# Kernel optimization log

Hardware: AMD Instinct MI355X
Metric: run time of the kernel (lower is better)

Reference implementation:

```python
import jax, jax.numpy as jnp
import numpy as np

TEMP = 5.0      # torch_kmeans SoftKMeans default temperature
N_ITERS = 25    # fixed iteration count (tolerance-based stop removed for jit)
EPS = 1e-9


def _soft_kmeans(x, l, key):
    # x: (r, q, d) -> labels (r, q) int32, centers (r, l, d)
    r, q, d = x.shape
    keys = jax.random.split(key, r)
    # random-point init (one permutation per batch, first l points)
    idx = jax.vmap(lambda k: jax.random.permutation(k, q)[:l])(keys)  # (r, l)
    centers = jnp.take_along_axis(x, idx[:, :, None], axis=1)         # (r, l, d)
    x_sq = jnp.sum(x * x, axis=-1)                                    # (r, q)

    def dist_to(centers):
        # squared euclidean distance (r, q, l)
        return (x_sq[:, :, None]
                - 2.0 * jnp.einsum('rqd,rld->rql', x, centers)
                + jnp.sum(centers * centers, axis=-1)[:, None, :])

    def step(centers, _):
        w = jax.nn.softmax(-TEMP * dist_to(centers), axis=-1)         # (r, q, l)
        denom = jnp.sum(w, axis=1)[:, :, None] + EPS                  # (r, l, 1)
        centers = jnp.einsum('rql,rqd->rld', w, x) / denom
        return centers, None

    centers, _ = jax.lax.scan(step, centers, None, length=N_ITERS)
    labels = jnp.argmin(dist_to(centers), axis=-1)                    # (r, q)
    return labels, centers


def setup_inputs() -> dict:
    key = jax.random.key(0)
    x = jax.random.normal(key, (8, 2048, 1024), dtype=jnp.float32)
    return {"x": x, "q": 4096, "r": 8, "l": 256}


def reference(x, q, r, l):
    B, T, F = x.shape
    # B*T*F must equal r*q*d; mirrors x.view(B,-1).view(B,q,-1).view(r,q,-1)
    xr = x.reshape(r, q, -1)
    labels, centers = _soft_kmeans(xr, l, jax.random.key(42))
    # gather centroid per point: rec[b, i, :] = centers[b, labels[b, i], :]
    rec = jnp.take_along_axis(centers, labels[:, :, None], axis=1)    # (r, q, d)
    return rec.reshape(B, T, F)
```

## Files before the change

kernel.cpp:

```cpp
#include <hip/hip_runtime.h>
#include <stdint.h>

#define RB 8
#define QN 4096
#define DN 512
#define LN 256
#define NITERS 25

typedef double f64x4 __attribute__((ext_vector_type(4)));

__device__ __forceinline__ void tf2x32(uint32_t k0, uint32_t k1,
                                       uint32_t x0, uint32_t x1,
                                       uint32_t& y0, uint32_t& y1) {
  uint32_t ks2 = k0 ^ k1 ^ 0x1BD11BDAu;
#define TFR(r) { x0 += x1; x1 = (x1 << (r)) | (x1 >> (32 - (r))); x1 ^= x0; }
  x0 += k0; x1 += k1;
  TFR(13) TFR(15) TFR(26) TFR(6)   x0 += k1;  x1 += ks2 + 1u;
  TFR(17) TFR(29) TFR(16) TFR(24)  x0 += ks2; x1 += k0 + 2u;
  TFR(13) TFR(15) TFR(26) TFR(6)   x0 += k0;  x1 += k1 + 3u;
  TFR(17) TFR(29) TFR(16) TFR(24)  x0 += k1;  x1 += ks2 + 4u;
  TFR(13) TFR(15) TFR(26) TFR(6)   x0 += ks2; x1 += k0 + 5u;
#undef TFR
  y0 = x0; y1 = x1;
}
// ... 79 lines not shown
  f64x4 acc = {0.0, 0.0, 0.0, 0.0};
#pragma unroll
  for (int kk = 0; kk < 4; kk++) {
    double a  = xT[kk * 4 + kg][li];
    double bv = cT[kk * 4 + kg][li];
    acc = __builtin_amdgcn_mfma_f64_16x16x4f64(a, bv, acc, 0, 0, 0);
  }
  bool ok1 = true, ok2 = true;
#pragma unroll
  for (int d = 0; d < 4; d++) {
    int q1 = kg * 4 + d;
    int q2 = kg + 4 * d;
    double ref1 = 0.0, ref2 = 0.0;
    for (int dd = 0; dd < 16; dd++) {
      ref1 += xT[dd][q1] * cT[dd][li];
      ref2 += xT[dd][q2] * cT[dd][li];
    }
    ok1 = ok1 && (acc[d] == ref1);
    ok2 = ok2 && (acc[d] == ref2);
  }
  unsigned long long v1 = __ballot(ok1);
  unsigned long long v2 = __ballot(ok2);
  if (t == 0) *flag = (v1 == ~0ull) ? 1 : ((v2 == ~0ull) ? 2 : 0);
}

#define QT 64
#define XPD 69
#define CPD 261
#define DK 16
#define XLD 82
#define CLDf 260
__device__ __forceinline__ int grow(int q) { return q + ((q >> 3) << 1); }

#define ARENA_D 5920

__global__ __launch_bounds__(256, 2) void k_assign(const float* __restrict__ x,
                                                   const float* __restrict__ centers,
                                                   const double* __restrict__ csqd,
                                                   float* __restrict__ W,
                                                   const int* __restrict__ flag) {
  __shared__ double arena[ARENA_D];
  const int mode = *flag;
  const int b = blockIdx.y, q0 = blockIdx.x * QT, t = threadIdx.x;
  const float* xb = x + ((size_t)b * QN + q0) * DN;
  const float* cb = centers + (size_t)b * LN * DN;
  const int xrow = t >> 2, xc4 = t & 3;

  if (mode != 0) {
    double (*xT)[XPD]  = (double(*)[XPD])arena;
    double (*cT)[CPD]  = (double(*)[CPD])(arena + 16 * XPD);
    double (*redm)[5]  = (double(*)[5])(arena + 16 * XPD + 16 * CPD);
    double (*reds)[5]  = (double(*)[5])(arena + 16 * XPD + 16 * CPD + 320);
    const int w = t >> 6, lane = t & 63;
    const int kg = lane >> 4, li = lane & 15;

    f64x4 acc[4][4];
#pragma unroll
    for (int i = 0; i < 4; i++)
#pragma unroll
      for (int j = 0; j < 4; j++) acc[i][j] = (f64x4){0.0, 0.0, 0.0, 0.0};

    float4 gx, gc[4];
    gx = *(const float4*)(xb + (size_t)xrow * DN + xc4 * 4);
#pragma unroll
    for (int i = 0; i < 4; i++) {
      int f = t + 256 * i; int row = f >> 2, c4 = f & 3;
      gc[i] = *(const float4*)(cb + (size_t)row * DN + c4 * 4);
    }

    for (int d0 = 0; d0 < DN; d0 += 16) {
      xT[xc4 * 4 + 0][xrow] = (double)gx.x;
      xT[xc4 * 4 + 1][xrow] = (double)gx.y;
      xT[xc4 * 4 + 2][xrow] = (double)gx.z;
      xT[xc4 * 4 + 3][xrow] = (double)gx.w;
#pragma unroll
      for (int i = 0; i < 4; i++) {
        int f = t + 256 * i; int row = f >> 2, c4 = f & 3;
        cT[c4 * 4 + 0][row] = (double)gc[i].x;
        cT[c4 * 4 + 1][row] = (double)gc[i].y;
        cT[c4 * 4 + 2][row] = (double)gc[i].z;
        cT[c4 * 4 + 3][row] = (double)gc[i].w;
      }
      __syncthreads();
      if (d0 + 16 < DN) {
        gx = *(const float4*)(xb + (size_t)xrow * DN + (d0 + 16) + xc4 * 4);
#pragma unroll
        for (int i = 0; i < 4; i++) {
          int f = t + 256 * i; int row = f >> 2, c4 = f & 3;
          gc[i] = *(const float4*)(cb + (size_t)row * DN + (d0 + 16) + c4 * 4);
        }
      }
      double a0[4], b0[4];
#pragma unroll
      for (int qt = 0; qt < 4; qt++) a0[qt] = xT[kg][qt * 16 + li];
#pragma unroll
      for (int lt = 0; lt < 4; lt++) b0[lt] = cT[kg][w * 64 + lt * 16 + li];
#pragma unroll
      for (int kk = 0; kk < 4; kk++) {
        double a1[4], b1[4];
        if (kk + 1 < 4) {
#pragma unroll
          for (int qt = 0; qt < 4; qt++) a1[qt] = xT[(kk + 1) * 4 + kg][qt * 16 + li];
#pragma unroll
          for (int lt = 0; lt < 4; lt++) b1[lt] = cT[(kk + 1) * 4 + kg][w * 64 + lt * 16 + li];
        }
#pragma unroll
        for (int qt = 0; qt < 4; qt++)
#pragma unroll
          for (int lt = 0; lt < 4; lt++)
            acc[qt][lt] = __builtin_amdgcn_mfma_f64_16x16x4f64(a0[qt], b0[lt], acc[qt][lt], 0, 0, 0);
        if (kk + 1 < 4) {
#pragma unroll
          for (int qt = 0; qt < 4; qt++) a0[qt] = a1[qt];
#pragma unroll
          for (int lt = 0; lt < 4; lt++) b0[lt] = b1[lt];
        }
      }
      __syncthreads();
    }

    double csqv[4];
#pragma unroll
    for (int lt = 0; lt < 4; lt++) csqv[lt] = csqd[b * LN + w * 64 + lt * 16 + li];

    double rm[4][4];
#pragma unroll
    for (int qt = 0; qt < 4; qt++)
#pragma unroll
      for (int d = 0; d < 4; d++) {
        double m = -1e300;
#pragma unroll
        for (int lt = 0; lt < 4; lt++) {
          double lg = -5.0 * (csqv[lt] - 2.0 * acc[qt][lt][d]);
          acc[qt][lt][d] = lg;
          m = fmax(m, lg);
        }
        rm[qt][d] = m;
      }
#pragma unroll
    for (int off = 1; off < 16; off <<= 1)
#pragma unroll
      for (int qt = 0; qt < 4; qt++)
#pragma unroll
        for (int d = 0; d < 4; d++) rm[qt][d] = fmax(rm[qt][d], __shfl_xor(rm[qt][d], off, 64));
    if (li == 0) {
#pragma unroll
      for (int qt = 0; qt < 4; qt++)
#pragma unroll
        for (int d = 0; d < 4; d++) {
          int qr = qt * 16 + ((mode == 1) ? (kg * 4 + d) : (kg + 4 * d));
          redm[qr][w] = rm[qt][d];
        }
    }
    __syncthreads();
#pragma unroll
    for (int qt = 0; qt < 4; qt++)
#pragma unroll
      for (int d = 0; d < 4; d++) {
        int qr = qt * 16 + ((mode == 1) ? (kg * 4 + d) : (kg + 4 * d));
        rm[qt][d] = fmax(fmax(redm[qr][0], redm[qr][1]), fmax(redm[qr][2], redm[qr][3]));
      }
    double sv[4][4];
#pragma unroll
    for (int qt = 0; qt < 4; qt++)
#pragma unroll
      for (int d = 0; d < 4; d++) {
        double s = 0.0;
#pragma unroll
        for (int lt = 0; lt < 4; lt++) {
          double e = exp(acc[qt][lt][d] - rm[qt][d]);
          acc[qt][lt][d] = e;
          s += e;
        }
        sv[qt][d] = s;
      }
#pragma unroll
    for (int off = 1; off < 16; off <<= 1)
#pragma unroll
      for (int qt = 0; qt < 4; qt++)
#pragma unroll
        for (int d = 0; d < 4; d++) sv[qt][d] += __shfl_xor(sv[qt][d], off, 64);
    if (li == 0) {
#pragma unroll
      for (int qt = 0; qt < 4; qt++)
#pragma unroll
        for (int d = 0; d < 4; d++) {
          int qr = qt * 16 + ((mode == 1) ? (kg * 4 + d) : (kg + 4 * d));
          reds[qr][w] = sv[qt][d];
        }
    }
    __syncthreads();
#pragma unroll
    for (int qt = 0; qt < 4; qt++)
#pragma unroll
      for (int d = 0; d < 4; d++) {
        int qr = qt * 16 + ((mode == 1) ? (kg * 4 + d) : (kg + 4 * d));
        double tot = reds[qr][0] + reds[qr][1] + reds[qr][2] + reds[qr][3];
        double inv = 1.0 / tot;
        float* wr = W + ((size_t)b * QN + q0 + qr) * LN + w * 64 + li;
#pragma unroll
        for (int lt = 0; lt < 4; lt++)
          wr[lt * 16] = (float)(acc[qt][lt][d] * inv);
      }
  } else {
    double (*xsD)[XLD]  = (double(*)[XLD])arena;
    float  (*csF)[CLDf] = (float(*)[CLDf])(arena + 16 * XLD);
    double (*red)[33]   = (double(*)[33])(arena + 16 * XLD + (16 * CLDf) / 2);
    const int rg = t & 7, cg = t >> 3;
    double acc[8][8];
#pragma unroll
    for (int i = 0; i < 8; i++)
#pragma unroll
      for (int j = 0; j < 8; j++) acc[i][j] = 0.0;

    const int xg = grow(xrow);
    float4 gx, gc[4];
    gx = *(const float4*)(xb + (size_t)xrow * DN + xc4 * 4);
#pragma unroll
    for (int i = 0; i < 4; i++) {
      int f = t + 256 * i; int row = f >> 2, c4 = f & 3;
      gc[i] = *(const float4*)(cb + (size_t)row * DN + c4 * 4);
    }

    for (int d0 = 0; d0 < DN; d0 += DK) {
      xsD[xc4 * 4 + 0][xg] = (double)gx.x; xsD[xc4 * 4 + 1][xg] = (double)gx.y;
      xsD[xc4 * 4 + 2][xg] = (double)gx.z; xsD[xc4 * 4 + 3][xg] = (double)gx.w;
#pragma unroll
      for (int i = 0; i < 4; i++) {
        int f = t + 256 * i; int row = f >> 2, c4 = f & 3;
        csF[c4 * 4 + 0][row] = gc[i].x; csF[c4 * 4 + 1][row] = gc[i].y;
        csF[c4 * 4 + 2][row] = gc[i].z; csF[c4 * 4 + 3][row] = gc[i].w;
      }
      __syncthreads();
      if (d0 + DK < DN) {
        gx = *(const float4*)(xb + (size_t)xrow * DN + (d0 + DK) + xc4 * 4);
#pragma unroll
        for (int i = 0; i < 4; i++) {
          int f = t + 256 * i; int row = f >> 2, c4 = f & 3;
          gc[i] = *(const float4*)(cb + (size_t)row * DN + (d0 + DK) + c4 * 4);
        }
      }
      double xva[8]; float4 ca0, ca1;
#pragma unroll
      for (int j = 0; j < 8; j++) xva[j] = xsD[0][rg * 10 + j];
      ca0 = *(const float4*)&csF[0][cg * 8];
      ca1 = *(const float4*)&csF[0][cg * 8 + 4];
#pragma unroll
      for (int k = 0; k < DK; k++) {
        double xvb[8]; float4 cb0, cb1;
        if (k + 1 < DK) {
#pragma unroll
          for (int j = 0; j < 8; j++) xvb[j] = xsD[k + 1][rg * 10 + j];
          cb0 = *(const float4*)&csF[k + 1][cg * 8];
          cb1 = *(const float4*)&csF[k + 1][cg * 8 + 4];
        }
        double cv[8] = {(double)ca0.x, (double)ca0.y, (double)ca0.z, (double)ca0.w,
                        (double)ca1.x, (double)ca1.y, (double)ca1.z, (double)ca1.w};
#pragma unroll
        for (int i = 0; i < 8; i++)
#pragma unroll
          for (int j = 0; j < 8; j++)
            acc[i][j] = fma(xva[i], cv[j], acc[i][j]);
        if (k + 1 < DK) {
#pragma unroll
          for (int j = 0; j < 8; j++) xva[j] = xvb[j];
          ca0 = cb0; ca1 = cb1;
        }
      }
      __syncthreads();
    }

    double csqv[8];
#pragma unroll
    for (int j = 0; j < 8; j++) csqv[j] = csqd[b * LN + cg * 8 + j];

    double lmax[8];
#pragma unroll
    for (int i = 0; i < 8; i++) {
      double m = -1e300;
#pragma unroll
      for (int j = 0; j < 8; j++) {
        double lg = -5.0 * (csqv[j] - 2.0 * acc[i][j]);
        acc[i][j] = lg;
        m = fmax(m, lg);
      }
      lmax[i] = m;
    }
#pragma unroll
    for (int i = 0; i < 8; i++) red[rg * 8 + i][cg] = lmax[i];
    __syncthreads();
    double rmax[8];
#pragma unroll
    for (int i = 0; i < 8; i++) {
      double m = -1e300;
      for (int c = 0; c < 32; c++) m = fmax(m, red[rg * 8 + i][c]);
      rmax[i] = m;
    }
    __syncthreads();
#pragma unroll
    for (int i = 0; i < 8; i++) {
      double s = 0.0;
#pragma unroll
      for (int j = 0; j < 8; j++) {
        double e = exp(acc[i][j] - rmax[i]);
        acc[i][j] = e;
        s += e;
      }
      red[rg * 8 + i][cg] = s;
    }
    __syncthreads();
#pragma unroll
    for (int i = 0; i < 8; i++) {
      double s = 0.0;
      for (int c = 0; c < 32; c++) s += red[rg * 8 + i][c];
      float* wrow = W + ((size_t)b * QN + q0 + rg * 8 + i) * LN + cg * 8;
      float4 v0 = make_float4((float)(acc[i][0] / s), (float)(acc[i][1] / s),
                              (float)(acc[i][2] / s), (float)(acc[i][3] / s));
      float4 v1 = make_float4((float)(acc[i][4] / s), (float)(acc[i][5] / s),
                              (float)(acc[i][6] / s), (float)(acc[i][7] / s));
      *(float4*)wrow = v0;
      *(float4*)(wrow + 4) = v1;
    }
  }
}

#define NCH 8
#define CHQ (QN / NCH)
#define UKQ 16

__global__ __launch_bounds__(256, 3) void k_update_split(
    const float* __restrict__ W, const float* __restrict__ x,
    float* __restrict__ P, float* __restrict__ dsum) {
  __shared__ float wT[UKQ][132];
  __shared__ float xT[UKQ][132];
  const int b = blockIdx.z;
  const int s = blockIdx.y;
  const int lt = (blockIdx.x >> 2) * 128;
  const int dt = (blockIdx.x & 3) * 128;
  const int t = threadIdx.x;
  const int tr = t >> 4, tc = t & 15;
  float acc[8][8];
#pragma unroll
  for (int i = 0; i < 8; i++)
#pragma unroll
    for (int j = 0; j < 8; j++) acc[i][j] = 0.f;
  float dsm[8] = {0, 0, 0, 0, 0, 0, 0, 0};

  const float* Wb = W + ((size_t)b * QN + (size_t)s * CHQ) * LN + lt;
  const float* xb = x + ((size_t)b * QN + (size_t)s * CHQ) * DN + dt;

  float4 gw[2], gx2[2];
#pragma unroll
  for (int i = 0; i < 2; i++) {
    int f = t + 256 * i; int row = f >> 5, c = f & 31;
    gw[i]  = *(const float4*)(Wb + (size_t)row * LN + c * 4);
    gx2[i] = *(const float4*)(xb + (size_t)row * DN + c * 4);
  }

  for (int k0 = 0; k0 < CHQ; k0 += UKQ) {
#pragma unroll
    for (int i = 0; i < 2; i++) {
      int f = t + 256 * i; int row = f >> 5, c = f & 31;
      *(float4*)&wT[row][c * 4] = gw[i];
// ... 93 lines not shown
      int f = t + 256 * i;
      int row = f >> 4, c4 = f & 15;
      *(float4*)&wT[row][c4 * 4] = *(const float4*)(Wb + (size_t)(k0 + row) * LN + l0 + c4 * 4);
    }
#pragma unroll
    for (int i = 0; i < 2; i++) {
      int f = t + 256 * i;
      int row = f >> 4, c4 = f & 15;
      *(float4*)&xT[row][c4 * 4] = *(const float4*)(xb + (size_t)(k0 + row) * DN + d0 + c4 * 4);
    }
    __syncthreads();
#pragma unroll
    for (int k = 0; k < KQ; k++) {
      float wf[4], xf[4];
      *(float4*)wf = *(const float4*)&wT[k][rg * 4];
      *(float4*)xf = *(const float4*)&xT[k][cg * 4];
#pragma unroll
      for (int i = 0; i < 4; i++) {
        dsm[i] += wf[i];
#pragma unroll
        for (int j = 0; j < 4; j++) acc[i][j] = fmaf(wf[i], xf[j], acc[i][j]);
      }
    }
    __syncthreads();
  }
#pragma unroll
  for (int i = 0; i < 4; i++) {
    float den = dsm[i] + 1e-9f;
    *(float4*)(cnew + ((size_t)b * LN + l0 + rg * 4 + i) * DN + d0 + cg * 4) =
        make_float4(acc[i][0] / den, acc[i][1] / den, acc[i][2] / den, acc[i][3] / den);
  }
}

#define ARENA_F 6048
__global__ __launch_bounds__(256, 2) void k_final(const float* __restrict__ x,
                                                  const float* __restrict__ centers,
                                                  const double* __restrict__ csqd,
                                                  float* __restrict__ out,
                                                  const int* __restrict__ flag) {
  __shared__ double arena[ARENA_F];
  const int mode = *flag;
  const int b = blockIdx.y, q0 = blockIdx.x * QT, t = threadIdx.x;
  const float* xb = x + ((size_t)b * QN + q0) * DN;
  const float* cb = centers + (size_t)b * LN * DN;
  const int xrow = t >> 2, xc4 = t & 3;

  if (mode != 0) {
    double (*xT)[XPD] = (double(*)[XPD])arena;
    double (*cT)[CPD] = (double(*)[CPD])(arena + 16 * XPD);
    double (*redv)[5] = (double(*)[5])(arena + 16 * XPD + 16 * CPD);
    int*    redi      = (int*)(arena + 16 * XPD + 16 * CPD + 320);
    unsigned short* labels = (unsigned short*)(arena + 16 * XPD + 16 * CPD + 480);
    const int w = t >> 6, lane = t & 63;
    const int kg = lane >> 4, li = lane & 15;

    f64x4 acc[4][4];
#pragma unroll
    for (int i = 0; i < 4; i++)
#pragma unroll
      for (int j = 0; j < 4; j++) acc[i][j] = (f64x4){0.0, 0.0, 0.0, 0.0};

    float4 gx, gc[4];
    gx = *(const float4*)(xb + (size_t)xrow * DN + xc4 * 4);
#pragma unroll
    for (int i = 0; i < 4; i++) {
      int f = t + 256 * i; int row = f >> 2, c4 = f & 3;
      gc[i] = *(const float4*)(cb + (size_t)row * DN + c4 * 4);
    }

    for (int d0 = 0; d0 < DN; d0 += 16) {
      xT[xc4 * 4 + 0][xrow] = (double)gx.x;
      xT[xc4 * 4 + 1][xrow] = (double)gx.y;
      xT[xc4 * 4 + 2][xrow] = (double)gx.z;
      xT[xc4 * 4 + 3][xrow] = (double)gx.w;
#pragma unroll
      for (int i = 0; i < 4; i++) {
        int f = t + 256 * i; int row = f >> 2, c4 = f & 3;
        cT[c4 * 4 + 0][row] = (double)gc[i].x;
        cT[c4 * 4 + 1][row] = (double)gc[i].y;
        cT[c4 * 4 + 2][row] = (double)gc[i].z;
        cT[c4 * 4 + 3][row] = (double)gc[i].w;
      }
      __syncthreads();
      if (d0 + 16 < DN) {
        gx = *(const float4*)(xb + (size_t)xrow * DN + (d0 + 16) + xc4 * 4);
#pragma unroll
        for (int i = 0; i < 4; i++) {
          int f = t + 256 * i; int row = f >> 2, c4 = f & 3;
          gc[i] = *(const float4*)(cb + (size_t)row * DN + (d0 + 16) + c4 * 4);
        }
      }
      double a0[4], b0[4];
#pragma unroll
      for (int qt = 0; qt < 4; qt++) a0[qt] = xT[kg][qt * 16 + li];
#pragma unroll
      for (int lt = 0; lt < 4; lt++) b0[lt] = cT[kg][w * 64 + lt * 16 + li];
#pragma unroll
      for (int kk = 0; kk < 4; kk++) {
        double a1[4], b1[4];
        if (kk + 1 < 4) {
#pragma unroll
          for (int qt = 0; qt < 4; qt++) a1[qt] = xT[(kk + 1) * 4 + kg][qt * 16 + li];
#pragma unroll
          for (int lt = 0; lt < 4; lt++) b1[lt] = cT[(kk + 1) * 4 + kg][w * 64 + lt * 16 + li];
        }
#pragma unroll
        for (int qt = 0; qt < 4; qt++)
#pragma unroll
          for (int lt = 0; lt < 4; lt++)
            acc[qt][lt] = __builtin_amdgcn_mfma_f64_16x16x4f64(a0[qt], b0[lt], acc[qt][lt], 0, 0, 0);
        if (kk + 1 < 4) {
#pragma unroll
          for (int qt = 0; qt < 4; qt++) a0[qt] = a1[qt];
#pragma unroll
          for (int lt = 0; lt < 4; lt++) b0[lt] = b1[lt];
        }
      }
      __syncthreads();
    }

    double csqv[4];
#pragma unroll
    for (int lt = 0; lt < 4; lt++) csqv[lt] = csqd[b * LN + w * 64 + lt * 16 + li];

    double bv[4][4]; int bi[4][4];
#pragma unroll
    for (int qt = 0; qt < 4; qt++)
#pragma unroll
      for (int d = 0; d < 4; d++) {
        double best = 1e300; int bidx = 0;
#pragma unroll
        for (int lt = 0; lt < 4; lt++) {
          double dd = csqv[lt] - 2.0 * acc[qt][lt][d];
          int l = w * 64 + lt * 16 + li;
          if (dd < best) { best = dd; bidx = l; }
        }
        bv[qt][d] = best; bi[qt][d] = bidx;
      }
#pragma unroll
    for (int off = 1; off < 16; off <<= 1)
#pragma unroll
      for (int qt = 0; qt < 4; qt++)
#pragma unroll
        for (int d = 0; d < 4; d++) {
          double ov = __shfl_xor(bv[qt][d], off, 64);
          int oi = __shfl_xor(bi[qt][d], off, 64);
          if (ov < bv[qt][d] || (ov == bv[qt][d] && oi < bi[qt][d])) {
            bv[qt][d] = ov; bi[qt][d] = oi;
          }
        }
    if (li == 0) {
#pragma unroll
      for (int qt = 0; qt < 4; qt++)
#pragma unroll
        for (int d = 0; d < 4; d++) {
          int qr = qt * 16 + ((mode == 1) ? (kg * 4 + d) : (kg + 4 * d));
          redv[qr][w] = bv[qt][d];
          redi[qr * 5 + w] = bi[qt][d];
        }
    }
    __syncthreads();
    if (t < QT) {
      double best = redv[t][0]; int bidx = redi[t * 5 + 0];
#pragma unroll
      for (int ww = 1; ww < 4; ww++) {
        double v = redv[t][ww]; int id = redi[t * 5 + ww];
        if (v < best || (v == best && id < bidx)) { best = v; bidx = id; }
      }
      labels[t] = (unsigned short)bidx;
    }
    __syncthreads();
    const float4* cb4 = (const float4*)(centers + (size_t)b * LN * DN);
    float4* ob = (float4*)(out + ((size_t)b * QN + q0) * DN);
    for (int e = t; e < QT * (DN / 4); e += 256) {
      int row = e >> 7, c = e & 127;
      ob[(size_t)row * 128 + c] = cb4[(size_t)labels[row] * 128 + c];
    }
  } else {
    double (*xsD)[XLD]  = (double(*)[XLD])arena;
    float  (*csF)[CLDf] = (float(*)[CLDf])(arena + 16 * XLD);
    double (*redv)[33]  = (double(*)[33])(arena + 3392);
    unsigned short* redi = (unsigned short*)(arena + 5504);
    unsigned short* labels = (unsigned short*)(arena + 6032);
    const int rg = t & 7, cg = t >> 3;
    double acc[8][8];
#pragma unroll
    for (int i = 0; i < 8; i++)
#pragma unroll
      for (int j = 0; j < 8; j++) acc[i][j] = 0.0;

    const int xg = grow(xrow);
    float4 gx, gc[4];
    gx = *(const float4*)(xb + (size_t)xrow * DN + xc4 * 4);
#pragma unroll
    for (int i = 0; i < 4; i++) {
      int f = t + 256 * i; int row = f >> 2, c4 = f & 3;
      gc[i] = *(const float4*)(cb + (size_t)row * DN + c4 * 4);
    }

    for (int d0 = 0; d0 < DN; d0 += DK) {
      xsD[xc4 * 4 + 0][xg] = (double)gx.x; xsD[xc4 * 4 + 1][xg] = (double)gx.y;
      xsD[xc4 * 4 + 2][xg] = (double)gx.z; xsD[xc4 * 4 + 3][xg] = (double)gx.w;
#pragma unroll
      for (int i = 0; i < 4; i++) {
        int f = t + 256 * i; int row = f >> 2, c4 = f & 3;
        csF[c4 * 4 + 0][row] = gc[i].x; csF[c4 * 4 + 1][row] = gc[i].y;
        csF[c4 * 4 + 2][row] = gc[i].z; csF[c4 * 4 + 3][row] = gc[i].w;
      }
      __syncthreads();
      if (d0 + DK < DN) {
        gx = *(const float4*)(xb + (size_t)xrow * DN + (d0 + DK) + xc4 * 4);
#pragma unroll
        for (int i = 0; i < 4; i++) {
          int f = t + 256 * i; int row = f >> 2, c4 = f & 3;
          gc[i] = *(const float4*)(cb + (size_t)row * DN + (d0 + DK) + c4 * 4);
        }
      }
      double xva[8]; float4 ca0, ca1;
#pragma unroll
      for (int j = 0; j < 8; j++) xva[j] = xsD[0][rg * 10 + j];
      ca0 = *(const float4*)&csF[0][cg * 8];
      ca1 = *(const float4*)&csF[0][cg * 8 + 4];
#pragma unroll
      for (int k = 0; k < DK; k++) {
        double xvb[8]; float4 cb0, cb1;
        if (k + 1 < DK) {
#pragma unroll
          for (int j = 0; j < 8; j++) xvb[j] = xsD[k + 1][rg * 10 + j];
          cb0 = *(const float4*)&csF[k + 1][cg * 8];
          cb1 = *(const float4*)&csF[k + 1][cg * 8 + 4];
        }
        double cv[8] = {(double)ca0.x, (double)ca0.y, (double)ca0.z, (double)ca0.w,
                        (double)ca1.x, (double)ca1.y, (double)ca1.z, (double)ca1.w};
#pragma unroll
        for (int i = 0; i < 8; i++)
#pragma unroll
          for (int j = 0; j < 8; j++)
            acc[i][j] = fma(xva[i], cv[j], acc[i][j]);
        if (k + 1 < DK) {
#pragma unroll
          for (int j = 0; j < 8; j++) xva[j] = xvb[j];
          ca0 = cb0; ca1 = cb1;
        }
      }
      __syncthreads();
    }

    double csqv[8];
#pragma unroll
    for (int j = 0; j < 8; j++) csqv[j] = csqd[b * LN + cg * 8 + j];

    double bv[8]; int bi[8];
#pragma unroll
    for (int i = 0; i < 8; i++) {
      bv[i] = 1e300; bi[i] = 0;
#pragma unroll
      for (int j = 0; j < 8; j++) {
        double dd = csqv[j] - 2.0 * acc[i][j];
        if (dd < bv[i]) { bv[i] = dd; bi[i] = cg * 8 + j; }
      }
    }
#pragma unroll
    for (int i = 0; i < 8; i++) {
      redv[rg * 8 + i][cg] = bv[i];
      redi[(rg * 8 + i) * 33 + cg] = (unsigned short)bi[i];
    }
    __syncthreads();
    if (t < QT) {
      double best = 1e300; int bidx = 0;
      for (int c = 0; c < 32; c++) {
        double v = redv[t][c];
        int id = redi[t * 33 + c];
        if (v < best || (v == best && id < bidx)) { best = v; bidx = id; }
      }
      labels[t] = (unsigned short)bidx;
    }
    __syncthreads();
    const float4* cb4 = (const float4*)(centers + (size_t)b * LN * DN);
    float4* ob = (float4*)(out + ((size_t)b * QN + q0) * DN);
    for (int e = t; e < QT * (DN / 4); e += 256) {
      int row = e >> 7, c = e & 127;
      ob[(size_t)row * 128 + c] = cb4[(size_t)labels[row] * 128 + c];
    }
  }
}

extern "C" void kernel_launch(void* const* d_in, const int* in_sizes, int n_in,
                              void* d_out, int out_size, void* d_ws, size_t ws_size,
                              hipStream_t stream) {
  const float* x = (const float*)d_in[0];
  float* out = (float*)d_out;

  const size_t szC    = (size_t)RB * LN * DN * sizeof(float);
  const size_t szCsqD = (size_t)RB * LN * sizeof(double);
  const size_t szDsum = (size_t)NCH * RB * LN * sizeof(float);
  const size_t szFlag = 256;
  const size_t szW    = (size_t)RB * QN * LN * sizeof(float);

  char* p = (char*)d_ws;
  float*  cA   = (float*)p;  p += szC;
  float*  cB   = (float*)p;  p += szC;
  double* csqd = (double*)p; p += szCsqD;
  float*  dsum = (float*)p;  p += szDsum;
  int*    flag = (int*)p;    p += szFlag;
  const bool bigws = ws_size >= 2 * szC + szCsqD + szDsum + szFlag + szW;
  float* W = bigws ? (float*)p : (float*)d_out;
  float* P = (float*)d_out;

  k_probe<<<1, 64, 0, stream>>>(flag);
  k_init<<<RB, 1024, 0, stream>>>(x, cA);
  k_rowsq_d<<<(RB * LN) / 4, 256, 0, stream>>>(cA, csqd, RB * LN);

  float* cur = cA;
  float* nxt = cB;
  for (int it = 0; it < NITERS; ++it) {
    k_assign<<<dim3(QN / QT, RB), 256, 0, stream>>>(x, cur, csqd, W, flag);
    if (bigws) {
      k_update_split<<<dim3(8, NCH, RB), 256, 0, stream>>>(W, x, P, dsum);
      k_reduce<<<RB * LN, 128, 0, stream>>>(P, dsum, nxt, csqd);
    } else {
      k_update_mono<<<dim3(LN / LT, DN / DT, RB), 256, 0, stream>>>(W, x, nxt);
      k_rowsq_d<<<(RB * LN) / 4, 256, 0, stream>>>(nxt, csqd, RB * LN);
    }
    float* tmp = cur; cur = nxt; nxt = tmp;
  }
  k_final<<<dim3(QN / QT, RB), 256, 0, stream>>>(x, cur, csqd, out, flag);
}
```

Before: 7.589 ms.

## Use 512-thread blocks in assign/final kernels and double update split chunks

The MFMA path of k_assign and k_final now runs 8 wavefronts per block, each owning 32 centroid columns instead of 64. Tile loading and the cross-wave max/sum reductions are redistributed to match. The FP64 scalar fallback path is gated to the first 256 threads. Separately, k_update_split now splits the point dimension into 16 chunks instead of 8, with a higher occupancy hint. The aim is more waves per CU to hide latency and more parallelism in the update, at the cost of more shared-memory reduction traffic and more partial sums to combine.

New measurement: 12.72 ms. 1.68x slower.

```diff
diff --git a/kernel.cpp b/kernel.cpp
--- a/kernel.cpp
+++ b/kernel.cpp
@@ -135,9 +135,9 @@
 #define CLDf 260
 __device__ __forceinline__ int grow(int q) { return q + ((q >> 3) << 1); }
 
-#define ARENA_D 5920
-
-__global__ __launch_bounds__(256, 2) void k_assign(const float* __restrict__ x,
+#define ARENA_D 6432
+
+__global__ __launch_bounds__(512, 4) void k_assign(const float* __restrict__ x,
                                                    const float* __restrict__ centers,
                                                    const double* __restrict__ csqd,
                                                    float* __restrict__ W,
@@ -147,84 +147,76 @@
   const int b = blockIdx.y, q0 = blockIdx.x * QT, t = threadIdx.x;
   const float* xb = x + ((size_t)b * QN + q0) * DN;
   const float* cb = centers + (size_t)b * LN * DN;
-  const int xrow = t >> 2, xc4 = t & 3;
 
   if (mode != 0) {
-    double (*xT)[XPD]  = (double(*)[XPD])arena;
-    double (*cT)[CPD]  = (double(*)[CPD])(arena + 16 * XPD);
-    double (*redm)[5]  = (double(*)[5])(arena + 16 * XPD + 16 * CPD);
-    double (*reds)[5]  = (double(*)[5])(arena + 16 * XPD + 16 * CPD + 320);
+    double (*xT)[XPD] = (double(*)[XPD])arena;
+    double (*cT)[CPD] = (double(*)[CPD])(arena + 16 * XPD);
+    double (*redm)[9] = (double(*)[9])(arena + 16 * XPD + 16 * CPD);
+    double (*reds)[9] = (double(*)[9])(arena + 16 * XPD + 16 * CPD + 576);
     const int w = t >> 6, lane = t & 63;
     const int kg = lane >> 4, li = lane & 15;
-
-    f64x4 acc[4][4];
+    const int xrow = t >> 3, xc2 = t & 7;
+    const int crow = t >> 1, cc8 = t & 1;
+
+    f64x4 acc[4][2];
 #pragma unroll
     for (int i = 0; i < 4; i++)
 #pragma unroll
-      for (int j = 0; j < 4; j++) acc[i][j] = (f64x4){0.0, 0.0, 0.0, 0.0};
-
-    float4 gx, gc[4];
-    gx = *(const float4*)(xb + (size_t)xrow * DN + xc4 * 4);
-#pragma unroll
-    for (int i = 0; i < 4; i++) {
-      int f = t + 256 * i; int row = f >> 2, c4 = f & 3;
-      gc[i] = *(const float4*)(cb + (size_t)row * DN + c4 * 4);
-    }
+      for (int j = 0; j < 2; j++) acc[i][j] = (f64x4){0.0, 0.0, 0.0, 0.0};
+
+    float2 gx = *(const float2*)(xb + (size_t)xrow * DN + xc2 * 2);
+    float4 gc0 = *(const float4*)(cb + (size_t)crow * DN + cc8 * 8);
+    float4 gc1 = *(const float4*)(cb + (size_t)crow * DN + cc8 * 8 + 4);
 
     for (int d0 = 0; d0 < DN; d0 += 16) {
-      xT[xc4 * 4 + 0][xrow] = (double)gx.x;
-      xT[xc4 * 4 + 1][xrow] = (double)gx.y;
-      xT[xc4 * 4 + 2][xrow] = (double)gx.z;
-      xT[xc4 * 4 + 3][xrow] = (double)gx.w;
-#pragma unroll
-      for (int i = 0; i < 4; i++) {
-        int f = t + 256 * i; int row = f >> 2, c4 = f & 3;
-        cT[c4 * 4 + 0][row] = (double)gc[i].x;
-        cT[c4 * 4 + 1][row] = (double)gc[i].y;
-        cT[c4 * 4 + 2][row] = (double)gc[i].z;
-        cT[c4 * 4 + 3][row] = (double)gc[i].w;
-      }
+      xT[xc2 * 2 + 0][xrow] = (double)gx.x;
+      xT[xc2 * 2 + 1][xrow] = (double)gx.y;
+      cT[cc8 * 8 + 0][crow] = (double)gc0.x;
+      cT[cc8 * 8 + 1][crow] = (double)gc0.y;
+      cT[cc8 * 8 + 2][crow] = (double)gc0.z;
+      cT[cc8 * 8 + 3][crow] = (double)gc0.w;
+      cT[cc8 * 8 + 4][crow] = (double)gc1.x;
+      cT[cc8 * 8 + 5][crow] = (double)gc1.y;
+      cT[cc8 * 8 + 6][crow] = (double)gc1.z;
+      cT[cc8 * 8 + 7][crow] = (double)gc1.w;
       __syncthreads();
       if (d0 + 16 < DN) {
-        gx = *(const float4*)(xb + (size_t)xrow * DN + (d0 + 16) + xc4 * 4);
-#pragma unroll
-        for (int i = 0; i < 4; i++) {
-          int f = t + 256 * i; int row = f >> 2, c4 = f & 3;
-          gc[i] = *(const float4*)(cb + (size_t)row * DN + (d0 + 16) + c4 * 4);
-        }
-      }
-      double a0[4], b0[4];
+        gx  = *(const float2*)(xb + (size_t)xrow * DN + (d0 + 16) + xc2 * 2);
+        gc0 = *(const float4*)(cb + (size_t)crow * DN + (d0 + 16) + cc8 * 8);
+        gc1 = *(const float4*)(cb + (size_t)crow * DN + (d0 + 16) + cc8 * 8 + 4);
+      }
+      double a0[4], b0[2];
 #pragma unroll
       for (int qt = 0; qt < 4; qt++) a0[qt] = xT[kg][qt * 16 + li];
 #pragma unroll
-      for (int lt = 0; lt < 4; lt++) b0[lt] = cT[kg][w * 64 + lt * 16 + li];
+      for (int lt = 0; lt < 2; lt++) b0[lt] = cT[kg][w * 32 + lt * 16 + li];
 #pragma unroll
       for (int kk = 0; kk < 4; kk++) {
-        double a1[4], b1[4];
+        double a1[4], b1[2];
         if (kk + 1 < 4) {
 #pragma unroll
           for (int qt = 0; qt < 4; qt++) a1[qt] = xT[(kk + 1) * 4 + kg][qt * 16 + li];
 #pragma unroll
-          for (int lt = 0; lt < 4; lt++) b1[lt] = cT[(kk + 1) * 4 + kg][w * 64 + lt * 16 + li];
+          for (int lt = 0; lt < 2; lt++) b1[lt] = cT[(kk + 1) * 4 + kg][w * 32 + lt * 16 + li];
         }
 #pragma unroll
         for (int qt = 0; qt < 4; qt++)
 #pragma unroll
-          for (int lt = 0; lt < 4; lt++)
+          for (int lt = 0; lt < 2; lt++)
             acc[qt][lt] = __builtin_amdgcn_mfma_f64_16x16x4f64(a0[qt], b0[lt], acc[qt][lt], 0, 0, 0);
         if (kk + 1 < 4) {
 #pragma unroll
           for (int qt = 0; qt < 4; qt++) a0[qt] = a1[qt];
 #pragma unroll
-          for (int lt = 0; lt < 4; lt++) b0[lt] = b1[lt];
+          for (int lt = 0; lt < 2; lt++) b0[lt] = b1[lt];
         }
       }
       __syncthreads();
     }
 
-    double csqv[4];
-#pragma unroll
-    for (int lt = 0; lt < 4; lt++) csqv[lt] = csqd[b * LN + w * 64 + lt * 16 + li];
+    double csqv[2];
+#pragma unroll
+    for (int lt = 0; lt < 2; lt++) csqv[lt] = csqd[b * LN + w * 32 + lt * 16 + li];
 
     double rm[4][4];
 #pragma unroll
@@ -233,7 +225,7 @@
       for (int d = 0; d < 4; d++) {
         double m = -1e300;
 #pragma unroll
-        for (int lt = 0; lt < 4; lt++) {
+        for (int lt = 0; lt < 2; lt++) {
           double lg = -5.0 * (csqv[lt] - 2.0 * acc[qt][lt][d]);
           acc[qt][lt][d] = lg;
           m = fmax(m, lg);
@@ -261,7 +253,10 @@
 #pragma unroll
       for (int d = 0; d < 4; d++) {
         int qr = qt * 16 + ((mode == 1) ? (kg * 4 + d) : (kg + 4 * d));
-        rm[qt][d] = fmax(fmax(redm[qr][0], redm[qr][1]), fmax(redm[qr][2], redm[qr][3]));
+        double m = redm[qr][0];
+#pragma unroll
+        for (int ww = 1; ww < 8; ww++) m = fmax(m, redm[qr][ww]);
+        rm[qt][d] = m;
       }
     double sv[4][4];
 #pragma unroll
@@ -270,7 +265,7 @@
       for (int d = 0; d < 4; d++) {
         double s = 0.0;
 #pragma unroll
-        for (int lt = 0; lt < 4; lt++) {
+        for (int lt = 0; lt < 2; lt++) {
           double e = exp(acc[qt][lt][d] - rm[qt][d]);
           acc[qt][lt][d] = e;
           s += e;
@@ -293,145 +288,162 @@
         }
     }
     __syncthreads();
+    const size_t qbase = (size_t)b * QN + q0;
 #pragma unroll
     for (int qt = 0; qt < 4; qt++)
 #pragma unroll
       for (int d = 0; d < 4; d++) {
         int qr = qt * 16 + ((mode == 1) ? (kg * 4 + d) : (kg + 4 * d));
-        double tot = reds[qr][0] + reds[qr][1] + reds[qr][2] + reds[qr][3];
+        double tot = 0.0;
+#pragma unroll
+        for (int ww = 0; ww < 8; ww++) tot += reds[qr][ww];
         double inv = 1.0 / tot;
-        float* wr = W + ((size_t)b * QN + q0 + qr) * LN + w * 64 + li;
-#pragma unroll
-        for (int lt = 0; lt < 4; lt++)
-          wr[lt * 16] = (float)(acc[qt][lt][d] * inv);
+        float* wr = W + (qbase + qr) * LN + w * 32 + li;
+        wr[0]  = (float)(acc[qt][0][d] * inv);
+        wr[16] = (float)(acc[qt][1][d] * inv);
       }
   } else {
+    const bool act = t < 256;
+    const int t2 = t & 255;
     double (*xsD)[XLD]  = (double(*)[XLD])arena;
     float  (*csF)[CLDf] = (float(*)[CLDf])(arena + 16 * XLD);
     double (*red)[33]   = (double(*)[33])(arena + 16 * XLD + (16 * CLDf) / 2);
-    const int rg = t & 7, cg = t >> 3;
+    const int rg = t2 & 7, cg = t2 >> 3;
+    const int xrow = t2 >> 2, xc4 = t2 & 3;
+    const int xg = grow(xrow);
     double acc[8][8];
 #pragma unroll
     for (int i = 0; i < 8; i++)
 #pragma unroll
       for (int j = 0; j < 8; j++) acc[i][j] = 0.0;
 
-    const int xg = grow(xrow);
-    float4 gx, gc[4];
-    gx = *(const float4*)(xb + (size_t)xrow * DN + xc4 * 4);
-#pragma unroll
-    for (int i = 0; i < 4; i++) {
-      int f = t + 256 * i; int row = f >> 2, c4 = f & 3;
-      gc[i] = *(const float4*)(cb + (size_t)row * DN + c4 * 4);
+    float4 gx = make_float4(0, 0, 0, 0), gc[4];
+    if (act) {
+      gx = *(const float4*)(xb + (size_t)xrow * DN + xc4 * 4);
+#pragma unroll
+      for (int i = 0; i < 4; i++) {
+        int f = t2 + 256 * i; int row = f >> 2, c4 = f & 3;
+        gc[i] = *(const float4*)(cb + (size_t)row * DN + c4 * 4);
+      }
     }
 
     for (int d0 = 0; d0 < DN; d0 += DK) {
-      xsD[xc4 * 4 + 0][xg] = (double)gx.x; xsD[xc4 * 4 + 1][xg] = (double)gx.y;
-      xsD[xc4 * 4 + 2][xg] = (double)gx.z; xsD[xc4 * 4 + 3][xg] = (double)gx.w;
-#pragma unroll
-      for (int i = 0; i < 4; i++) {
-        int f = t + 256 * i; int row = f >> 2, c4 = f & 3;
-        csF[c4 * 4 + 0][row] = gc[i].x; csF[c4 * 4 + 1][row] = gc[i].y;
-        csF[c4 * 4 + 2][row] = gc[i].z; csF[c4 * 4 + 3][row] = gc[i].w;
+      if (act) {
+        xsD[xc4 * 4 + 0][xg] = (double)gx.x; xsD[xc4 * 4 + 1][xg] = (double)gx.y;
+        xsD[xc4 * 4 + 2][xg] = (double)gx.z; xsD[xc4 * 4 + 3][xg] = (double)gx.w;
+#pragma unroll
+        for (int i = 0; i < 4; i++) {
+          int f = t2 + 256 * i; int row = f >> 2, c4 = f & 3;
+          csF[c4 * 4 + 0][row] = gc[i].x; csF[c4 * 4 + 1][row] = gc[i].y;
+          csF[c4 * 4 + 2][row] = gc[i].z; csF[c4 * 4 + 3][row] = gc[i].w;
+        }
       }
       __syncthreads();
-      if (d0 + DK < DN) {
-        gx = *(const float4*)(xb + (size_t)xrow * DN + (d0 + DK) + xc4 * 4);
-#pragma unroll
-        for (int i = 0; i < 4; i++) {
-          int f = t + 256 * i; int row = f >> 2, c4 = f & 3;
-          gc[i] = *(const float4*)(cb + (size_t)row * DN + (d0 + DK) + c4 * 4);
-        }
-      }
-      double xva[8]; float4 ca0, ca1;
-#pragma unroll
-      for (int j = 0; j < 8; j++) xva[j] = xsD[0][rg * 10 + j];
-      ca0 = *(const float4*)&csF[0][cg * 8];
-      ca1 = *(const float4*)&csF[0][cg * 8 + 4];
-#pragma unroll
-      for (int k = 0; k < DK; k++) {
-        double xvb[8]; float4 cb0, cb1;
-        if (k + 1 < DK) {
-#pragma unroll
-          for (int j = 0; j < 8; j++) xvb[j] = xsD[k + 1][rg * 10 + j];
-          cb0 = *(const float4*)&csF[k + 1][cg * 8];
-          cb1 = *(const float4*)&csF[k + 1][cg * 8 + 4];
-        }
-        double cv[8] = {(double)ca0.x, (double)ca0.y, (double)ca0.z, (double)ca0.w,
-                        (double)ca1.x, (double)ca1.y, (double)ca1.z, (double)ca1.w};
-#pragma unroll
-        for (int i = 0; i < 8; i++)
-#pragma unroll
-          for (int j = 0; j < 8; j++)
-            acc[i][j] = fma(xva[i], cv[j], acc[i][j]);
-        if (k + 1 < DK) {
-#pragma unroll
-          for (int j = 0; j < 8; j++) xva[j] = xvb[j];
-          ca0 = cb0; ca1 = cb1;
+      if (act) {
+        if (d0 + DK < DN) {
+          gx = *(const float4*)(xb + (size_t)xrow * DN + (d0 + DK) + xc4 * 4);
+#pragma unroll
+          for (int i = 0; i < 4; i++) {
+            int f = t2 + 256 * i; int row = f >> 2, c4 = f & 3;
+            gc[i] = *(const float4*)(cb + (size_t)row * DN + (d0 + DK) + c4 * 4);
+          }
+        }
+        double xva[8]; float4 ca0, ca1;
+#pragma unroll
+        for (int j = 0; j < 8; j++) xva[j] = xsD[0][rg * 10 + j];
+        ca0 = *(const float4*)&csF[0][cg * 8];
+        ca1 = *(const float4*)&csF[0][cg * 8 + 4];
+#pragma unroll
+        for (int k = 0; k < DK; k++) {
+          double xvb[8]; float4 cb0, cb1;
+          if (k + 1 < DK) {
+#pragma unroll
+            for (int j = 0; j < 8; j++) xvb[j] = xsD[k + 1][rg * 10 + j];
+            cb0 = *(const float4*)&csF[k + 1][cg * 8];
+            cb1 = *(const float4*)&csF[k + 1][cg * 8 + 4];
+          }
+          double cv[8] = {(double)ca0.x, (double)ca0.y, (double)ca0.z, (double)ca0.w,
+                          (double)ca1.x, (double)ca1.y, (double)ca1.z, (double)ca1.w};
+#pragma unroll
+          for (int i = 0; i < 8; i++)
+#pragma unroll
+            for (int j = 0; j < 8; j++)
+              acc[i][j] = fma(xva[i], cv[j], acc[i][j]);
+          if (k + 1 < DK) {
+#pragma unroll
+            for (int j = 0; j < 8; j++) xva[j] = xvb[j];
+            ca0 = cb0; ca1 = cb1;
+          }
         }
       }
       __syncthreads();
     }
 
-    double csqv[8];
-#pragma unroll
-    for (int j = 0; j < 8; j++) csqv[j] = csqd[b * LN + cg * 8 + j];
-
-    double lmax[8];
-#pragma unroll
-    for (int i = 0; i < 8; i++) {
-      double m = -1e300;
-#pragma unroll
-      for (int j = 0; j < 8; j++) {
-        double lg = -5.0 * (csqv[j] - 2.0 * acc[i][j]);
-        acc[i][j] = lg;
-        m = fmax(m, lg);
-      }
-      lmax[i] = m;
-    }
-#pragma unroll
-    for (int i = 0; i < 8; i++) red[rg * 8 + i][cg] = lmax[i];
+    double csqv[8], lmax[8];
+    if (act) {
+#pragma unroll
+      for (int j = 0; j < 8; j++) csqv[j] = csqd[b * LN + cg * 8 + j];
+#pragma unroll
+      for (int i = 0; i < 8; i++) {
+        double m = -1e300;
+#pragma unroll
+        for (int j = 0; j < 8; j++) {
+          double lg = -5.0 * (csqv[j] - 2.0 * acc[i][j]);
+          acc[i][j] = lg;
+          m = fmax(m, lg);
+        }
+        lmax[i] = m;
+      }
+#pragma unroll
+      for (int i = 0; i < 8; i++) red[rg * 8 + i][cg] = lmax[i];
+    }
     __syncthreads();
     double rmax[8];
-#pragma unroll
-    for (int i = 0; i < 8; i++) {
-      double m = -1e300;
-      for (int c = 0; c < 32; c++) m = fmax(m, red[rg * 8 + i][c]);
-      rmax[i] = m;
-    }
-    __syncthreads();
-#pragma unroll
-    for (int i = 0; i < 8; i++) {
-      double s = 0.0;
-#pragma unroll
-      for (int j = 0; j < 8; j++) {
-        double e = exp(acc[i][j] - rmax[i]);
-        acc[i][j] = e;
-        s += e;
-      }
-      red[rg * 8 + i][cg] = s;
-    }
-    __syncthreads();
-#pragma unroll
-    for (int i = 0; i < 8; i++) {
-      double s = 0.0;
-      for (int c = 0; c < 32; c++) s += red[rg * 8 + i][c];
-      float* wrow = W + ((size_t)b * QN + q0 + rg * 8 + i) * LN + cg * 8;
-      float4 v0 = make_float4((float)(acc[i][0] / s), (float)(acc[i][1] / s),
-                              (float)(acc[i][2] / s), (float)(acc[i][3] / s));
-      float4 v1 = make_float4((float)(acc[i][4] / s), (float)(acc[i][5] / s),
-                              (float)(acc[i][6] / s), (float)(acc[i][7] / s));
-      *(float4*)wrow = v0;
-      *(float4*)(wrow + 4) = v1;
+    if (act) {
+#pragma unroll
+      for (int i = 0; i < 8; i++) {
+        double m = -1e300;
+        for (int c = 0; c < 32; c++) m = fmax(m, red[rg * 8 + i][c]);
+        rmax[i] = m;
+      }
+    }
+    __syncthreads();
+    if (act) {
+#pragma unroll
+      for (int i = 0; i < 8; i++) {
+        double s = 0.0;
+#pragma unroll
+        for (int j = 0; j < 8; j++) {
+          double e = exp(acc[i][j] - rmax[i]);
+          acc[i][j] = e;
+          s += e;
+        }
+        red[rg * 8 + i][cg] = s;
+      }
+    }
+    __syncthreads();
+    if (act) {
+#pragma unroll
+      for (int i = 0; i < 8; i++) {
+        double s = 0.0;
+        for (int c = 0; c < 32; c++) s += red[rg * 8 + i][c];
+        float* wrow = W + ((size_t)b * QN + q0 + rg * 8 + i) * LN + cg * 8;
+        float4 v0 = make_float4((float)(acc[i][0] / s), (float)(acc[i][1] / s),
+                                (float)(acc[i][2] / s), (float)(acc[i][3] / s));
+        float4 v1 = make_float4((float)(acc[i][4] / s), (float)(acc[i][5] / s),
+                                (float)(acc[i][6] / s), (float)(acc[i][7] / s));
+        *(float4*)wrow = v0;
+        *(float4*)(wrow + 4) = v1;
+      }
     }
   }
 }
 
-#define NCH 8
+#define NCH 16
 #define CHQ (QN / NCH)
 #define UKQ 16
 
-__global__ __launch_bounds__(256, 3) void k_update_split(
+__global__ __launch_bounds__(256, 4) void k_update_split(
     const float* __restrict__ W, const float* __restrict__ x,
     float* __restrict__ P, float* __restrict__ dsum) {
   __shared__ float wT[UKQ][132];
@@ -591,96 +603,87 @@
   }
 }
 
-#define ARENA_F 6048
-__global__ __launch_bounds__(256, 2) void k_final(const float* __restrict__ x,
+__global__ __launch_bounds__(512, 4) void k_final(const float* __restrict__ x,
                                                   const float* __restrict__ centers,
                                                   const double* __restrict__ csqd,
                                                   float* __restrict__ out,
                                                   const int* __restrict__ flag) {
-  __shared__ double arena[ARENA_F];
+  __shared__ double arena[ARENA_D];
   const int mode = *flag;
   const int b = blockIdx.y, q0 = blockIdx.x * QT, t = threadIdx.x;
   const float* xb = x + ((size_t)b * QN + q0) * DN;
   const float* cb = centers + (size_t)b * LN * DN;
-  const int xrow = t >> 2, xc4 = t & 3;
 
   if (mode != 0) {
     double (*xT)[XPD] = (double(*)[XPD])arena;
     double (*cT)[CPD] = (double(*)[CPD])(arena + 16 * XPD);
-    double (*redv)[5] = (double(*)[5])(arena + 16 * XPD + 16 * CPD);
-    int*    redi      = (int*)(arena + 16 * XPD + 16 * CPD + 320);
-    unsigned short* labels = (unsigned short*)(arena + 16 * XPD + 16 * CPD + 480);
+    double (*redv)[9] = (double(*)[9])(arena + 16 * XPD + 16 * CPD);
+    int*    redi      = (int*)(arena + 16 * XPD + 16 * CPD + 576);
+    unsigned short* labels = (unsigned short*)(arena + 16 * XPD + 16 * CPD + 576 + 288);
     const int w = t >> 6, lane = t & 63;
     const int kg = lane >> 4, li = lane & 15;
-
-    f64x4 acc[4][4];
+    const int xrow = t >> 3, xc2 = t & 7;
+    const int crow = t >> 1, cc8 = t & 1;
+
+    f64x4 acc[4][2];
 #pragma unroll
     for (int i = 0; i < 4; i++)
 #pragma unroll
-      for (int j = 0; j < 4; j++) acc[i][j] = (f64x4){0.0, 0.0, 0.0, 0.0};
-
-    float4 gx, gc[4];
-    gx = *(const float4*)(xb + (size_t)xrow * DN + xc4 * 4);
-#pragma unroll
-    for (int i = 0; i < 4; i++) {
-      int f = t + 256 * i; int row = f >> 2, c4 = f & 3;
-      gc[i] = *(const float4*)(cb + (size_t)row * DN + c4 * 4);
-    }
+      for (int j = 0; j < 2; j++) acc[i][j] = (f64x4){0.0, 0.0, 0.0, 0.0};
+
+    float2 gx = *(const float2*)(xb + (size_t)xrow * DN + xc2 * 2);
+    float4 gc0 = *(const float4*)(cb + (size_t)crow * DN + cc8 * 8);
+    float4 gc1 = *(const float4*)(cb + (size_t)crow * DN + cc8 * 8 + 4);
 
     for (int d0 = 0; d0 < DN; d0 += 16) {
-      xT[xc4 * 4 + 0][xrow] = (double)gx.x;
-      xT[xc4 * 4 + 1][xrow] = (double)gx.y;
-      xT[xc4 * 4 + 2][xrow] = (double)gx.z;
-      xT[xc4 * 4 + 3][xrow] = (double)gx.w;
-#pragma unroll
-      for (int i = 0; i < 4; i++) {
-        int f = t + 256 * i; int row = f >> 2, c4 = f & 3;
-        cT[c4 * 4 + 0][row] = (double)gc[i].x;
-        cT[c4 * 4 + 1][row] = (double)gc[i].y;
-        cT[c4 * 4 + 2][row] = (double)gc[i].z;
-        cT[c4 * 4 + 3][row] = (double)gc[i].w;
-      }
+      xT[xc2 * 2 + 0][xrow] = (double)gx.x;
+      xT[xc2 * 2 + 1][xrow] = (double)gx.y;
+      cT[cc8 * 8 + 0][crow] = (double)gc0.x;
+      cT[cc8 * 8 + 1][crow] = (double)gc0.y;
+      cT[cc8 * 8 + 2][crow] = (double)gc0.z;
+      cT[cc8 * 8 + 3][crow] = (double)gc0.w;
+      cT[cc8 * 8 + 4][crow] = (double)gc1.x;
+      cT[cc8 * 8 + 5][crow] = (double)gc1.y;
+      cT[cc8 * 8 + 6][crow] = (double)gc1.z;
+      cT[cc8 * 8 + 7][crow] = (double)gc1.w;
       __syncthreads();
       if (d0 + 16 < DN) {
-        gx = *(const float4*)(xb + (size_t)xrow * DN + (d0 + 16) + xc4 * 4);
-#pragma unroll
-        for (int i = 0; i < 4; i++) {
-          int f = t + 256 * i; int row = f >> 2, c4 = f & 3;
-          gc[i] = *(const float4*)(cb + (size_t)row * DN + (d0 + 16) + c4 * 4);
-        }
-      }
-      double a0[4], b0[4];
+        gx  = *(const float2*)(xb + (size_t)xrow * DN + (d0 + 16) + xc2 * 2);
+        gc0 = *(const float4*)(cb + (size_t)crow * DN + (d0 + 16) + cc8 * 8);
+        gc1 = *(const float4*)(cb + (size_t)crow * DN + (d0 + 16) + cc8 * 8 + 4);
+      }
+      double a0[4], b0[2];
 #pragma unroll
       for (int qt = 0; qt < 4; qt++) a0[qt] = xT[kg][qt * 16 + li];
 #pragma unroll
-      for (int lt = 0; lt < 4; lt++) b0[lt] = cT[kg][w * 64 + lt * 16 + li];
+      for (int lt = 0; lt < 2; lt++) b0[lt] = cT[kg][w * 32 + lt * 16 + li];
 #pragma unroll
       for (int kk = 0; kk < 4; kk++) {
-        double a1[4], b1[4];
+        double a1[4], b1[2];
         if (kk + 1 < 4) {
 #pragma unroll
           for (int qt = 0; qt < 4; qt++) a1[qt] = xT[(kk + 1) * 4 + kg][qt * 16 + li];
 #pragma unroll
-          for (int lt = 0; lt < 4; lt++) b1[lt] = cT[(kk + 1) * 4 + kg][w * 64 + lt * 16 + li];
+          for (int lt = 0; lt < 2; lt++) b1[lt] = cT[(kk + 1) * 4 + kg][w * 32 + lt * 16 + li];
         }
 #pragma unroll
         for (int qt = 0; qt < 4; qt++)
 #pragma unroll
-          for (int lt = 0; lt < 4; lt++)
+          for (int lt = 0; lt < 2; lt++)
             acc[qt][lt] = __builtin_amdgcn_mfma_f64_16x16x4f64(a0[qt], b0[lt], acc[qt][lt], 0, 0, 0);
         if (kk + 1 < 4) {
 #pragma unroll
           for (int qt = 0; qt < 4; qt++) a0[qt] = a1[qt];
 #pragma unroll
-          for (int lt = 0; lt < 4; lt++) b0[lt] = b1[lt];
+          for (int lt = 0; lt < 2; lt++) b0[lt] = b1[lt];
         }
       }
       __syncthreads();
     }
 
-    double csqv[4];
-#pragma unroll
-    for (int lt = 0; lt < 4; lt++) csqv[lt] = csqd[b * LN + w * 64 + lt * 16 + li];
+    double csqv[2];
+#pragma unroll
+    for (int lt = 0; lt < 2; lt++) csqv[lt] = csqd[b * LN + w * 32 + lt * 16 + li];
 
     double bv[4][4]; int bi[4][4];
 #pragma unroll
@@ -689,9 +692,9 @@
       for (int d = 0; d < 4; d++) {
         double best = 1e300; int bidx = 0;
 #pragma unroll
-        for (int lt = 0; lt < 4; lt++) {
+        for (int lt = 0; lt < 2; lt++) {
           double dd = csqv[lt] - 2.0 * acc[qt][lt][d];
-          int l = w * 64 + lt * 16 + li;
+          int l = w * 32 + lt * 16 + li;
           if (dd < best) { best = dd; bidx = l; }
         }
         bv[qt][d] = best; bi[qt][d] = bidx;
@@ -715,15 +718,15 @@
         for (int d = 0; d < 4; d++) {
           int qr = qt * 16 + ((mode == 1) ? (kg * 4 + d) : (kg + 4 * d));
           redv[qr][w] = bv[qt][d];
-          redi[qr * 5 + w] = bi[qt][d];
+          redi[qr * 9 + w] = bi[qt][d];
         }
     }
     __syncthreads();
     if (t < QT) {
-      double best = redv[t][0]; int bidx = redi[t * 5 + 0];
-#pragma unroll
-      for (int ww = 1; ww < 4; ww++) {
-        double v = redv[t][ww]; int id = redi[t * 5 + ww];
+      double best = redv[t][0]; int bidx = redi[t * 9 + 0];
+#pragma unroll
+      for (int ww = 1; ww < 8; ww++) {
+        double v = redv[t][ww]; int id = redi[t * 9 + ww];
         if (v < best || (v == best && id < bidx)) { best = v; bidx = id; }
       }
       labels[t] = (unsigned short)bidx;
@@ -731,98 +734,108 @@
     __syncthreads();
     const float4* cb4 = (const float4*)(centers + (size_t)b * LN * DN);
     float4* ob = (float4*)(out + ((size_t)b * QN + q0) * DN);
-    for (int e = t; e < QT * (DN / 4); e += 256) {
+    for (int e = t; e < QT * (DN / 4); e += 512) {
       int row = e >> 7, c = e & 127;
       ob[(size_t)row * 128 + c] = cb4[(size_t)labels[row] * 128 + c];
     }
   } else {
+    const bool act = t < 256;
+    const int t2 = t & 255;
     double (*xsD)[XLD]  = (double(*)[XLD])arena;
     float  (*csF)[CLDf] = (float(*)[CLDf])(arena + 16 * XLD);
     double (*redv)[33]  = (double(*)[33])(arena + 3392);
     unsigned short* redi = (unsigned short*)(arena + 5504);
     unsigned short* labels = (unsigned short*)(arena + 6032);
-    const int rg = t & 7, cg = t >> 3;
+    const int rg = t2 & 7, cg = t2 >> 3;
+    const int xrow = t2 >> 2, xc4 = t2 & 3;
+    const int xg = grow(xrow);
     double acc[8][8];
 #pragma unroll
     for (int i = 0; i < 8; i++)
 #pragma unroll
       for (int j = 0; j < 8; j++) acc[i][j] = 0.0;
 
-    const int xg = grow(xrow);
-    float4 gx, gc[4];
-    gx = *(const float4*)(xb + (size_t)xrow * DN + xc4 * 4);
-#pragma unroll
-    for (int i = 0; i < 4; i++) {
-      int f = t + 256 * i; int row = f >> 2, c4 = f & 3;
-      gc[i] = *(const float4*)(cb + (size_t)row * DN + c4 * 4);
+    float4 gx = make_float4(0, 0, 0, 0), gc[4];
+    if (act) {
+      gx = *(const float4*)(xb + (size_t)xrow * DN + xc4 * 4);
+#pragma unroll
+      for (int i = 0; i < 4; i++) {
+        int f = t2 + 256 * i; int row = f >> 2, c4 = f & 3;
+        gc[i] = *(const float4*)(cb + (size_t)row * DN + c4 * 4);
+      }
     }
 
     for (int d0 = 0; d0 < DN; d0 += DK) {
-      xsD[xc4 * 4 + 0][xg] = (double)gx.x; xsD[xc4 * 4 + 1][xg] = (double)gx.y;
-      xsD[xc4 * 4 + 2][xg] = (double)gx.z; xsD[xc4 * 4 + 3][xg] = (double)gx.w;
-#pragma unroll
-      for (int i = 0; i < 4; i++) {
-        int f = t + 256 * i; int row = f >> 2, c4 = f & 3;
-        csF[c4 * 4 + 0][row] = gc[i].x; csF[c4 * 4 + 1][row] = gc[i].y;
-        csF[c4 * 4 + 2][row] = gc[i].z; csF[c4 * 4 + 3][row] = gc[i].w;
+      if (act) {
+        xsD[xc4 * 4 + 0][xg] = (double)gx.x; xsD[xc4 * 4 + 1][xg] = (double)gx.y;
+        xsD[xc4 * 4 + 2][xg] = (double)gx.z; xsD[xc4 * 4 + 3][xg] = (double)gx.w;
+#pragma unroll
+        for (int i = 0; i < 4; i++) {
+          int f = t2 + 256 * i; int row = f >> 2, c4 = f & 3;
+          csF[c4 * 4 + 0][row] = gc[i].x; csF[c4 * 4 + 1][row] = gc[i].y;
+          csF[c4 * 4 + 2][row] = gc[i].z; csF[c4 * 4 + 3][row] = gc[i].w;
+        }
       }
       __syncthreads();
-      if (d0 + DK < DN) {
-        gx = *(const float4*)(xb + (size_t)xrow * DN + (d0 + DK) + xc4 * 4);
-#pragma unroll
-        for (int i = 0; i < 4; i++) {
-          int f = t + 256 * i; int row = f >> 2, c4 = f & 3;
-          gc[i] = *(const float4*)(cb + (size_t)row * DN + (d0 + DK) + c4 * 4);
-        }
-      }
-      double xva[8]; float4 ca0, ca1;
-#pragma unroll
-      for (int j = 0; j < 8; j++) xva[j] = xsD[0][rg * 10 + j];
-      ca0 = *(const float4*)&csF[0][cg * 8];
-      ca1 = *(const float4*)&csF[0][cg * 8 + 4];
-#pragma unroll
-      for (int k = 0; k < DK; k++) {
-        double xvb[8]; float4 cb0, cb1;
-        if (k + 1 < DK) {
-#pragma unroll
-          for (int j = 0; j < 8; j++) xvb[j] = xsD[k + 1][rg * 10 + j];
-          cb0 = *(const float4*)&csF[k + 1][cg * 8];
-          cb1 = *(const float4*)&csF[k + 1][cg * 8 + 4];
-        }
-        double cv[8] = {(double)ca0.x, (double)ca0.y, (double)ca0.z, (double)ca0.w,
-                        (double)ca1.x, (double)ca1.y, (double)ca1.z, (double)ca1.w};
-#pragma unroll
-        for (int i = 0; i < 8; i++)
-#pragma unroll
-          for (int j = 0; j < 8; j++)
-            acc[i][j] = fma(xva[i], cv[j], acc[i][j]);
-        if (k + 1 < DK) {
-#pragma unroll
-          for (int j = 0; j < 8; j++) xva[j] = xvb[j];
-          ca0 = cb0; ca1 = cb1;
+      if (act) {
+        if (d0 + DK < DN) {
+          gx = *(const float4*)(xb + (size_t)xrow * DN + (d0 + DK) + xc4 * 4);
+#pragma unroll
+          for (int i = 0; i < 4; i++) {
+            int f = t2 + 256 * i; int row = f >> 2, c4 = f & 3;
+            gc[i] = *(const float4*)(cb + (size_t)row * DN + (d0 + DK) + c4 * 4);
+          }
+        }
+        double xva[8]; float4 ca0, ca1;
+#pragma unroll
+        for (int j = 0; j < 8; j++) xva[j] = xsD[0][rg * 10 + j];
+        ca0 = *(const float4*)&csF[0][cg * 8];
+        ca1 = *(const float4*)&csF[0][cg * 8 + 4];
+#pragma unroll
+        for (int k = 0; k < DK; k++) {
+          double xvb[8]; float4 cb0, cb1;
+          if (k + 1 < DK) {
+#pragma unroll
+            for (int j = 0; j < 8; j++) xvb[j] = xsD[k + 1][rg * 10 + j];
+            cb0 = *(const float4*)&csF[k + 1][cg * 8];
+            cb1 = *(const float4*)&csF[k + 1][cg * 8 + 4];
+          }
+          double cv[8] = {(double)ca0.x, (double)ca0.y, (double)ca0.z, (double)ca0.w,
+                          (double)ca1.x, (double)ca1.y, (double)ca1.z, (double)ca1.w};
+#pragma unroll
+          for (int i = 0; i < 8; i++)
+#pragma unroll
+            for (int j = 0; j < 8; j++)
+              acc[i][j] = fma(xva[i], cv[j], acc[i][j]);
+          if (k + 1 < DK) {
+#pragma unroll
+            for (int j = 0; j < 8; j++) xva[j] = xvb[j];
+            ca0 = cb0; ca1 = cb1;
+          }
         }
       }
       __syncthreads();
     }
 
-    double csqv[8];
-#pragma unroll
-    for (int j = 0; j < 8; j++) csqv[j] = csqd[b * LN + cg * 8 + j];
-
-    double bv[8]; int bi[8];
-#pragma unroll
-    for (int i = 0; i < 8; i++) {
-      bv[i] = 1e300; bi[i] = 0;
-#pragma unroll
-      for (int j = 0; j < 8; j++) {
-        double dd = csqv[j] - 2.0 * acc[i][j];
-        if (dd < bv[i]) { bv[i] = dd; bi[i] = cg * 8 + j; }
-      }
-    }
-#pragma unroll
-    for (int i = 0; i < 8; i++) {
-      redv[rg * 8 + i][cg] = bv[i];
-      redi[(rg * 8 + i) * 33 + cg] = (unsigned short)bi[i];
+    if (act) {
+      double csqv[8];
+#pragma unroll
+      for (int j = 0; j < 8; j++) csqv[j] = csqd[b * LN + cg * 8 + j];
+      double bv[8]; int bi[8];
+#pragma unroll
+      for (int i = 0; i < 8; i++) {
+        bv[i] = 1e300; bi[i] = 0;
+#pragma unroll
+        for (int j = 0; j < 8; j++) {
+          double dd = csqv[j] - 2.0 * acc[i][j];
+          if (dd < bv[i]) { bv[i] = dd; bi[i] = cg * 8 + j; }
+        }
+      }
+#pragma unroll
+      for (int i = 0; i < 8; i++) {
+        redv[rg * 8 + i][cg] = bv[i];
+        redi[(rg * 8 + i) * 33 + cg] = (unsigned short)bi[i];
+      }
     }
     __syncthreads();
     if (t < QT) {
@@ -837,7 +850,7 @@
     __syncthreads();
     const float4* cb4 = (const float4*)(centers + (size_t)b * LN * DN);
     float4* ob = (float4*)(out + ((size_t)b * QN + q0) * DN);
-    for (int e = t; e < QT * (DN / 4); e += 256) {
+    for (int e = t; e < QT * (DN / 4); e += 512) {
       int row = e >> 7, c = e & 127;
       ob[(size_t)row * 128 + c] = cb4[(size_t)labels[row] * 128 + c];
     }
@@ -873,7 +886,7 @@
   float* cur = cA;
   float* nxt = cB;
   for (int it = 0; it < NITERS; ++it) {
-    k_assign<<<dim3(QN / QT, RB), 256, 0, stream>>>(x, cur, csqd, W, flag);
+    k_assign<<<dim3(QN / QT, RB), 512, 0, stream>>>(x, cur, csqd, W, flag);
     if (bigws) {
       k_update_split<<<dim3(8, NCH, RB), 256, 0, stream>>>(W, x, P, dsum);
       k_reduce<<<RB * LN, 128, 0, stream>>>(P, dsum, nxt, csqd);
@@ -883,5 +896,5 @@
     }
     float* tmp = cur; cur = nxt; nxt = tmp;
   }
-  k_final<<<dim3(QN / QT, RB), 256, 0, stream>>>(x, cur, csqd, out, flag);
+  k_final<<<dim3(QN / QT, RB), 512, 0, stream>>>(x, cur, csqd, out, flag);
 }
```
